# Kernel tuning notes

Hardware: AMD Instinct MI355X
Metric: run time of the kernel (lower is better)

The kernel has to match this reference:

```python
import jax, jax.numpy as jnp
import numpy as np

B, T, F = 256, 128, 256          # batch, input_len, feature_num (= input_size)
HID = [1024, 256]                # hidden_size per layer; HID[-1] must equal F
OUT_LEN = 12
NUM_LAYERS = 2


def setup_inputs() -> dict:
    key = jax.random.key(0)
    ks = jax.random.split(key, 16)
    ins = [F] + HID
    d = {"x": jax.random.normal(ks[0], (B, T, F), dtype=jnp.float32)}
    # Gate order along leading axis 0: [i, f, o, c]
    for j in range(NUM_LAYERS):
        si = 1.0 / np.sqrt(ins[j])
        sh = 1.0 / np.sqrt(HID[j])
        d[f"Wx{j}"] = jax.random.uniform(ks[1 + 4 * j], (4, ins[j], HID[j]), jnp.float32, -si, si)
        d[f"bx{j}"] = jax.random.uniform(ks[2 + 4 * j], (4, HID[j]), jnp.float32, -si, si)
        d[f"Wh{j}"] = jax.random.uniform(ks[3 + 4 * j], (4, HID[j], HID[j]), jnp.float32, -sh, sh)
        d[f"bh{j}"] = jax.random.uniform(ks[4 + 4 * j], (4, HID[j]), jnp.float32, -sh, sh)
    st = 1.0 / np.sqrt(T)
    d["Wout"] = jax.random.uniform(ks[10], (T, OUT_LEN), jnp.float32, -st, st)
    d["bout"] = jax.random.uniform(ks[11], (OUT_LEN,), jnp.float32, -st, st)
    return d


def _lstm_forward(x, Wx, bx, Wh, bh):
    """Stacked LSTM over time. x: (B,T,F). Returns (out_seq (B,T,HID[-1]), h_n list, c_n list)."""
    b = x.shape[0]
    h0 = tuple(jnp.zeros((b, h), x.dtype) for h in HID)
    c0 = tuple(jnp.zeros((b, h), x.dtype) for h in HID)

    def step(carry, x_t):
        hs, cs = carry
        inp = x_t
        new_hs, new_cs = [], []
        for j in range(NUM_LAYERS):
            # fused 4-gate matmuls: (B,in) x (4,in,H) -> (4,B,H)
            g = (jnp.einsum('bi,gih->gbh', inp, Wx[j]) + bx[j][:, None, :]
                 + jnp.einsum('bh,gho->gbo', hs[j], Wh[j]) + bh[j][:, None, :])
            it = jax.nn.sigmoid(g[0])
            ft = jax.nn.sigmoid(g[1])
            ot = jax.nn.sigmoid(g[2])
            c = ft * cs[j] + it * jnp.tanh(g[3])
            h = ot * jnp.tanh(c)
            new_hs.append(h)
            new_cs.append(c)
            inp = h
        return (tuple(new_hs), tuple(new_cs)), inp

    (h_n, c_n), out_seq = jax.lax.scan(step, (h0, c0), jnp.swapaxes(x, 0, 1))
    return jnp.swapaxes(out_seq, 0, 1), h_n, c_n  # (B,T,HID[-1])


def reference(x, Wx0, bx0, Wh0, bh0, Wx1, bx1, Wh1, bh1, Wout, bout):
    Wx = [Wx0, Wx1]; bx = [bx0, bx1]; Wh = [Wh0, Wh1]; bh = [bh0, bh1]
    out_seq, h_n, c_n = _lstm_forward(x, Wx, bx, Wh, bh)
    b = x.shape[0]
    # Faithful to torch: flat row-major view (B,T,F) -> (B,F,T), NOT a transpose
    out = out_seq.reshape(b, -1, T)                 # (B, F, T)
    out = out @ Wout + bout                          # (B, F, OUT_LEN)
    out = out.reshape(b, OUT_LEN, -1)                # (B, OUT_LEN, F)
    return (out, h_n[0], h_n[1], c_n[0], c_n[1])
```

## Files before the change

kernel.cpp:

```cpp
#include <hip/hip_runtime.h>
#include <hip/hip_bf16.h>

typedef unsigned short u16;
typedef unsigned int u32;
typedef unsigned long long u64;
typedef __attribute__((ext_vector_type(8))) short short8;
typedef __attribute__((ext_vector_type(4))) float f32x4;

#define NB 256
#define NT 512
#define TS 128

#define OFF_H0  786432
#define OFF_H1  1048576
#define OFF_C0  1114112
#define OFF_C1  1376256

#define WSO_W0F  0
#define WSO_W1F  (WSO_W0F + 10485760)
#define WSO_B0   (WSO_W1F + 2621440)
#define WSO_B1   (WSO_B0  + 16384)
#define WSO_BAR  (WSO_B1  + 4096)
#define BAR_DW   (4096 + 64)
#define WSO_H0   (WSO_BAR + BAR_DW*4)
#define H0SEQ_BYTES (129*524288)
#define WSO_H1   (WSO_H0 + H0SEQ_BYTES)
#define H1SEQ_BYTES (129*131072)
#define WS_NEED  (WSO_H1 + H1SEQ_BYTES)

#define LDS_XB   65536
#define LDS_B1   98304
#define LDS_SZ   139264

struct MP {
  const float* x;
  const u16*  W0F;
  const u16*  W1F;
  const float* b0;
  const float* b1;
  u16*  H0;
  u16*  H1;
  float* out;
  unsigned* bar;
};

__device__ __forceinline__ float sigm(float x){ return 1.f/(1.f+__expf(-x)); }
__device__ __forceinline__ float tanh_(float x){
  float t = __expf(-2.f*fabsf(x));
  float r = (1.f - t)/(1.f + t);
  return x < 0.f ? -r : r;
}
__device__ __forceinline__ u16 f2b(float v){
  __hip_bfloat16 h = __float2bfloat16(v);
  return *reinterpret_cast<u16*>(&h);
}
__device__ __forceinline__ float b2f(u16 u){
  u32 w = ((u32)u) << 16;
  return *reinterpret_cast<float*>(&w);
}
__device__ __forceinline__ void ast32(u16* p, u32 v){
  __hip_atomic_store((u32*)p, v, __ATOMIC_RELAXED, __HIP_MEMORY_SCOPE_AGENT);
}
__device__ __forceinline__ f32x4 MF(short8 a, short8 b, f32x4 c){
  return __builtin_amdgcn_mfma_f32_16x16x32_bf16(a, b, c, 0, 0, 0);
}
__device__ __forceinline__ void gll16(const void* g, void* l){
  __builtin_amdgcn_global_load_lds(
      (const __attribute__((address_space(1))) void*)g,
      (__attribute__((address_space(3))) void*)l, 16, 0, 0);
}

#define STRX(x) #x
#define PLOADO(dst, ptr, off) asm volatile("global_load_dwordx4 %0, %1, off offset:" STRX(off) : "=v"(dst) : "v"(ptr))
#define VMW(N)  do{ asm volatile("s_waitcnt vmcnt(" STRX(N) ")" ::: "memory"); __builtin_amdgcn_sched_barrier(0); }while(0)
#define BAR     do{ __builtin_amdgcn_s_barrier(); __builtin_amdgcn_sched_barrier(0); }while(0)


__global__ void k_packF0(const float* __restrict__ Wx, const float* __restrict__ Wh,
                         u16* __restrict__ W0F){
  int gid = blockIdx.x*256 + threadIdx.x;
  int F = gid >> 6, lane = gid & 63;
  int kk = F & 3, wn = (F >> 2) & 3;
  int r = F >> 4, kt = r % 10, nt = r / 10;
  int n = nt*64 + wn*16 + (lane & 15);
  int h = n >> 2, g = n & 3;
  int kb = kt*128 + kk*32 + (lane >> 4)*8;
  union { u16 u[8]; short8 v; } pk;
#pragma unroll
  for (int j = 0; j < 8; ++j) {
    int k = kb + j;
    float v = (k < 256) ? Wx[((size_t)g*256 + k)*1024 + h]
                        : Wh[((size_t)g*1024 + (k-256))*1024 + h];
    pk.u[j] = f2b(v);
  }
  *(short8*)&W0F[(size_t)F*512 + lane*8] = pk.v;
}

__global__ void k_packF1(const float* __restrict__ Wx, const float* __restrict__ Wh,
                         u16* __restrict__ W1F){
  int gid = blockIdx.x*256 + threadIdx.x;
  int F = gid >> 6, lane = gid & 63;
  int kk = F & 3, kt = (F >> 2) % 10, ntp = F / 40;
  int n = ntp*16 + (lane & 15);
  int h = n >> 2, g = n & 3;
  int kb = kt*128 + kk*32 + (lane >> 4)*8;
  union { u16 u[8]; short8 v; } pk;
#pragma unroll
  for (int j = 0; j < 8; ++j) {
    int k = kb + j;
    float v = (k < 1024) ? Wx[((size_t)g*1024 + k)*256 + h]
                         : Wh[((size_t)g*256 + (k-1024))*256 + h];
    pk.u[j] = f2b(v);
  }
  *(short8*)&W1F[(size_t)F*512 + lane*8] = pk.v;
}

__global__ void k_bias(const float* __restrict__ bx0, const float* __restrict__ bh0,
                       const float* __restrict__ bx1, const float* __restrict__ bh1,
                       float* __restrict__ b0, float* __restrict__ b1){
  int n = blockIdx.x*256 + threadIdx.x;
  if (n < 4096) { int h = n >> 2, g = n & 3; b0[n] = bx0[g*1024 + h] + bh0[g*1024 + h]; }
  if (n < 1024) { int h = n >> 2, g = n & 3; b1[n] = bx1[g*256 + h] + bh1[g*256 + h]; }
}

__global__ void k_init(u16* __restrict__ H0, u16* __restrict__ H1,
                       unsigned* __restrict__ bar){
  int i = blockIdx.x*256 + threadIdx.x;
  if (i < 262144) H0[i] = 0;
  if (i < 65536)  H1[i] = 0;
  if (i < BAR_DW) bar[i] = 0u;
}


__device__ __forceinline__ void xcvt(const MP& p, int g, char* smem){
  const int tid = threadIdx.x;
  const int row = tid >> 3, f0 = (tid & 7) << 5;
  const int m0 = (blockIdx.x >> 6) << 6;
  const float* xs = p.x + (size_t)(m0 + row)*32768 + (size_t)g*256 + f0;
  f32x4 v0,v1,v2,v3,v4,v5,v6,v7;
  PLOADO(v0, xs, 0);  PLOADO(v1, xs, 16); PLOADO(v2, xs, 32); PLOADO(v3, xs, 48);
  PLOADO(v4, xs, 64); PLOADO(v5, xs, 80); PLOADO(v6, xs, 96); PLOADO(v7, xs, 112);
  VMW(0);
  char* xb = smem + LDS_XB + ((f0 >> 7) << 14);
  const int cb = (f0 & 127) >> 3, sw = row & 7;
  union { u16 u[8]; short8 s; } pk;
#define XPK(VA, VB, CC) \
  pk.u[0]=f2b(VA[0]); pk.u[1]=f2b(VA[1]); pk.u[2]=f2b(VA[2]); pk.u[3]=f2b(VA[3]); \
  pk.u[4]=f2b(VB[0]); pk.u[5]=f2b(VB[1]); pk.u[6]=f2b(VB[2]); pk.u[7]=f2b(VB[3]); \
  *(short8*)(xb + row*256 + ((((cb+(CC)) ^ sw))<<4)) = pk.s;
  XPK(v0,v1,0) XPK(v2,v3,1) XPK(v4,v5,2) XPK(v6,v7,3)
#undef XPK
}

__device__ __forceinline__ void fused(const MP& p, int g, char* smem,
                                      float* c0, float* c1, short8* wp,
                                      bool doP0, bool doP1){
  const int bid = blockIdx.x, tid = threadIdx.x;
  const int grp = bid >> 6, nt = bid & 63;
  const int m0 = grp*64, n0 = nt*64, n1 = nt*16;
  const int lane = tid & 63, wid = tid >> 6;
  const int wm = wid >> 2, wn = wid & 3;
  const int lrow = lane & 15, kgrp = lane >> 4;
  const int sw = lrow & 7;
  const int r8 = lane >> 4, c16 = lane & 15;
  const int row0 = wid*8 + r8, row1 = wid*8 + 4 + r8;
  const char* Hp = (const char*)(p.H0 + (size_t)g*262144);
  const char* h0 = Hp + (size_t)(m0+row0)*2048 + ((c16 ^ (row0 & 7))<<4);
  const char* h1 = Hp + (size_t)(m0+row1)*2048 + ((c16 ^ (row1 & 7))<<4);
  const int gB = (g > 0) ? (g-1) : 0;
  const char* HB = (const char*)(p.H1 + (size_t)gB*65536);
  const char* hB0 = HB + (size_t)(m0+row0)*512 + ((c16 ^ (row0 & 7))<<4);
  const char* hB1 = HB + (size_t)(m0+row1)*512 + ((c16 ^ (row1 & 7))<<4);
  char* d0 = smem + wid*2048;
  char* d1 = smem + wid*2048 + 1024;
  const u16* bb = p.W0F + (size_t)nt*81920 + wn*2048 + lane*8;
  const char* b1p = smem + LDS_B1;

  short8 bx0,bx1,bx2,bx3, by0,by1,by2,by3;
  f32x4 acc0 = {0,0,0,0}, acc1 = {0,0,0,0};
  f32x4 accp = {0,0,0,0};

#define FS0(T) do{ const int _o = ((T)-2)*256, _bi = (((T)-2)&3)*16384; \
    gll16(h0 + _o, d0 + _bi); gll16(h1 + _o, d1 + _bi); }while(0)
#define FS1(T) do{ const int _o = ((T)-10)*256, _bi = (((T)-2)&3)*16384; \
    gll16(hB0 + _o, d0 + _bi); gll16(hB1 + _o, d1 + _bi); }while(0)
#define F_MFB(BP, B0_,B1_,B2_,B3_) do{ const char* _bp = (BP); short8 _a0,_a1; \
    const int _r0 = (wm*32 + lrow)*256, _r1 = _r0 + 16*256; \
    _a0 = *(const short8*)(_bp + _r0 + (((0+kgrp) ^ sw)<<4)); \
    _a1 = *(const short8*)(_bp + _r1 + (((0+kgrp) ^ sw)<<4)); \
    acc0 = MF(_a0,B0_,acc0); acc1 = MF(_a1,B0_,acc1); \
    _a0 = *(const short8*)(_bp + _r0 + (((4+kgrp) ^ sw)<<4)); \
    _a1 = *(const short8*)(_bp + _r1 + (((4+kgrp) ^ sw)<<4)); \
    acc0 = MF(_a0,B1_,acc0); acc1 = MF(_a1,B1_,acc1); \
    _a0 = *(const short8*)(_bp + _r0 + (((8+kgrp) ^ sw)<<4)); \
    _a1 = *(const short8*)(_bp + _r1 + (((8+kgrp) ^ sw)<<4)); \
    acc0 = MF(_a0,B2_,acc0); acc1 = MF(_a1,B2_,acc1); \
    _a0 = *(const short8*)(_bp + _r0 + (((12+kgrp) ^ sw)<<4)); \
    _a1 = *(const short8*)(_bp + _r1 + (((12+kgrp) ^ sw)<<4)); \
    acc0 = MF(_a0,B3_,acc0); acc1 = MF(_a1,B3_,acc1); }while(0)
#define F_MF1(BUFI, KT1) do{ const char* _bp = smem + (BUFI)*16384; \
    const int _ro = (wid*16 + lrow)*256; short8 _a, _b; \
    _a = *(const short8*)(_bp + _ro + (((0+kgrp) ^ sw)<<4)); \
    _b = *(const short8*)(b1p + (((KT1)*4+0)<<10) + lane*16); accp = MF(_a,_b,accp); \
    _a = *(const short8*)(_bp + _ro + (((4+kgrp) ^ sw)<<4)); \
    _b = *(const short8*)(b1p + (((KT1)*4+1)<<10) + lane*16); accp = MF(_a,_b,accp); \
    _a = *(const short8*)(_bp + _ro + (((8+kgrp) ^ sw)<<4)); \
    _b = *(const short8*)(b1p + (((KT1)*4+2)<<10) + lane*16); accp = MF(_a,_b,accp); \
    _a = *(const short8*)(_bp + _ro + (((12+kgrp) ^ sw)<<4)); \
    _b = *(const short8*)(b1p + (((KT1)*4+3)<<10) + lane*16); accp = MF(_a,_b,accp); }while(0)

  { const u16* _s = bb;
    PLOADO(bx0,_s,0); PLOADO(bx1,_s,1024); PLOADO(bx2,_s,2048); PLOADO(bx3,_s,3072); }
  { const u16* _s = bb + 8192;
    PLOADO(by0,_s,0); PLOADO(by1,_s,1024); PLOADO(by2,_s,2048); PLOADO(by3,_s,3072); }
  FS0(2); FS0(3); FS0(4); FS0(5);

  VMW(12); BAR; if (doP0) F_MFB(smem + LDS_XB,         bx0,bx1,bx2,bx3);
  VMW(8);  BAR; if (doP0) F_MFB(smem + LDS_XB + 16384, by0,by1,by2,by3);
  VMW(6); BAR; if (doP0) F_MFB(smem,         wp[0], wp[1], wp[2], wp[3]);
               if (doP1 && wid < 4) F_MF1(0, 0);  FS0(6);
  VMW(6); BAR; if (doP0) F_MFB(smem + 16384, wp[4], wp[5], wp[6], wp[7]);
               if (doP1 && wid < 4) F_MF1(1, 1);  FS0(7);
  VMW(6); BAR; if (doP0) F_MFB(smem + 32768, wp[8], wp[9], wp[10], wp[11]);
               if (doP1 && wid < 4) F_MF1(2, 2);  FS0(8);
  VMW(6); BAR; if (doP0) F_MFB(smem + 49152, wp[12], wp[13], wp[14], wp[15]);
               if (doP1 && wid < 4) F_MF1(3, 3);  FS0(9);
  VMW(6); BAR; if (doP0) F_MFB(smem,         wp[16], wp[17], wp[18], wp[19]);
               if (doP1 && wid < 4) F_MF1(0, 4);  FS1(10);
  VMW(6); BAR; if (doP0) F_MFB(smem + 16384, wp[20], wp[21], wp[22], wp[23]);
               if (doP1 && wid < 4) F_MF1(1, 5);  FS1(11);
  VMW(6); BAR; if (doP0) F_MFB(smem + 32768, wp[24], wp[25], wp[26], wp[27]);
               if (doP1 && wid < 4) F_MF1(2, 6);
  VMW(4); BAR; if (doP0) F_MFB(smem + 49152, wp[28], wp[29], wp[30], wp[31]);
               if (doP1 && wid < 4) F_MF1(3, 7);
  VMW(2); BAR; if (doP1 && wid < 4) F_MF1(0, 8);
  VMW(0); BAR; if (doP1 && wid < 4) F_MF1(1, 9);

  __syncthreads();
  float* gl0 = (float*)smem;
  float* gl1 = (float*)(smem + 20480);
  if (doP0) {
#pragma unroll
    for (int r = 0; r < 4; ++r) {
      gl0[(wm*32      + kgrp*4 + r)*68 + wn*16 + lrow] = acc0[r];
      gl0[(wm*32 + 16 + kgrp*4 + r)*68 + wn*16 + lrow] = acc1[r];
    }
  }
  if (doP1 && wid < 4) {
#pragma unroll
    for (int r = 0; r < 4; ++r)
      gl1[(wid*16 + kgrp*4 + r)*20 + lrow] = accp[r];
  }
  __syncthreads();
  if (doP0) {
    u16* H0w = p.H0 + (size_t)(g+1)*262144;
    int bl = tid >> 3, hp = tid & 7;
    int b = m0 + bl, h = nt*16 + hp*2;
    float hn[2];
#pragma unroll
    for (int q = 0; q < 2; ++q) {
      int col = (hp*2 + q)*4;
      float gi = gl0[bl*68 + col+0] + p.b0[n0 + col+0];
      float gf = gl0[bl*68 + col+1] + p.b0[n0 + col+1];
      float go = gl0[bl*68 + col+2] + p.b0[n0 + col+2];
      float gc = gl0[bl*68 + col+3] + p.b0[n0 + col+3];
      float cn = sigm(gf)*c0[q] + sigm(gi)*tanh_(gc);
      hn[q] = sigm(go)*tanh_(cn);
      c0[q] = cn;
      if (g == TS-1) {
        p.out[OFF_H0 + (size_t)b*1024 + h + q] = hn[q];
        p.out[OFF_C0 + (size_t)b*1024 + h + q] = cn;
      }
    }
    ast32(H0w + (size_t)b*1024 + h, (u32)f2b(hn[0]) | ((u32)f2b(hn[1]) << 16));
  }
  if (doP1 && tid < 128) {
    u16* H1w = p.H1 + (size_t)g*65536;
    int bl = tid >> 1, hp = tid & 1;
    int b = m0 + bl, h = nt*4 + hp*2;
    float hn[2];
#pragma unroll
    for (int q = 0; q < 2; ++q) {
      int col = (hp*2 + q)*4;
      float gi = gl1[bl*20 + col+0] + p.b1[n1 + col+0];
      float gf = gl1[bl*20 + col+1] + p.b1[n1 + col+1];
      float go = gl1[bl*20 + col+2] + p.b1[n1 + col+2];
      float gc = gl1[bl*20 + col+3] + p.b1[n1 + col+3];
      float cn = sigm(gf)*c1[q] + sigm(gi)*tanh_(gc);
      hn[q] = sigm(go)*tanh_(cn);
      c1[q] = cn;
      if (g == TS) {
        p.out[OFF_H1 + (size_t)b*256 + h + q] = hn[q];
        p.out[OFF_C1 + (size_t)b*256 + h + q] = cn;
      }
    }
    ast32(H1w + (size_t)b*256 + h, (u32)f2b(hn[0]) | ((u32)f2b(hn[1]) << 16));
  }
}

__global__ __launch_bounds__(NT, 1) void k_main(MP p){
  __shared__ __attribute__((aligned(16))) char smem[LDS_SZ];
  float c0[2] = {0.f, 0.f};
  float c1[2] = {0.f, 0.f};
  short8 wp[32];
  const int bid = blockIdx.x, tid = threadIdx.x;
  const int grp = bid >> 6, j = bid & 63;
  const int lane = tid & 63, wid = tid >> 6;
  unsigned* flags = p.bar;
  unsigned* rel   = p.bar + 4096 + grp*16;

  {
    const char* wsrc = (const char*)p.W1F + (size_t)j*40960 + lane*16;
#pragma unroll
    for (int q = 0; q < 5; ++q) {
      int f = wid*5 + q;
      gll16(wsrc + f*1024, smem + LDS_B1 + f*1024);
    }
    VMW(0);
  }
  {
    const u16* bb = p.W0F + (size_t)j*81920 + (wid & 3)*2048 + lane*8;
#define LDW(T) do{ const u16* _s = bb + (size_t)(T)*8192; \
    PLOADO(wp[((T)-2)*4+0],_s,0); PLOADO(wp[((T)-2)*4+1],_s,1024); \
    PLOADO(wp[((T)-2)*4+2],_s,2048); PLOADO(wp[((T)-2)*4+3],_s,3072); }while(0)
    LDW(2); LDW(3); LDW(4); LDW(5); LDW(6); LDW(7); LDW(8); LDW(9);
#undef LDW
    VMW(0);
  }

  xcvt(p, 0, smem);
  __syncthreads();
  fused(p, 0, smem, c0, c1, wp, true, false);

  for (int g = 1; g <= TS; ++g) {
    __syncthreads();
    if (j == 0) {
      if (tid >= 1 && tid < 64) {
        while (__hip_atomic_load(&flags[(grp*64 + tid)*16], __ATOMIC_RELAXED,
                                 __HIP_MEMORY_SCOPE_AGENT) < (unsigned)g)
          __builtin_amdgcn_s_sleep(1);
      }
      __syncthreads();
      if (tid == 0)
        __hip_atomic_store(rel, (unsigned)g, __ATOMIC_RELAXED, __HIP_MEMORY_SCOPE_AGENT);
    } else {
      if (tid == 0)
        __hip_atomic_store(&flags[bid*16], (unsigned)g, __ATOMIC_RELAXED,
                           __HIP_MEMORY_SCOPE_AGENT);
    }
    if (g < TS) xcvt(p, g, smem);
    if (j != 0 && tid == 0) {
      while (__hip_atomic_load(rel, __ATOMIC_RELAXED, __HIP_MEMORY_SCOPE_AGENT) < (unsigned)g)
        __builtin_amdgcn_s_sleep(1);
    }
    __syncthreads();
    fused(p, g, smem, c0, c1, wp, g < TS, true);
  }
}

__global__ void k_final_seq(const u16* __restrict__ H1seq, const float* __restrict__ Wout,
                            const float* __restrict__ bout, float* __restrict__ out){
  __shared__ float Ws[1536];
  __shared__ float bs[12];
  for (int i = threadIdx.x; i < 1536; i += 256) Ws[i] = Wout[i];
  if (threadIdx.x < 12) bs[threadIdx.x] = bout[threadIdx.x];
  __syncthreads();
  int gid = blockIdx.x*256 + threadIdx.x;
  int b = gid >> 8, ii = gid & 255;
  const u16* src = H1seq + (size_t)((ii >> 1) + 1)*65536 + b*256 + (ii & 1)*128;
  float acc[12];
#pragma unroll
  for (int k = 0; k < 12; ++k) acc[k] = bs[k];
  for (int jj = 0; jj < 128; jj += 8) {
    union { u16 u[8]; short8 v; } pk;
    pk.v = *(const short8*)&src[jj];
#pragma unroll
    for (int e = 0; e < 8; ++e) {
      float f = b2f(pk.u[e]);
#pragma unroll
      for (int k = 0; k < 12; ++k) acc[k] += f*Ws[(jj+e)*12+k];
    }
  }
  float* dst = out + (size_t)b*3072 + ii*12;
#pragma unroll
  for (int k = 0; k < 12; ++k) dst[k] = acc[k];
}

extern "C" void kernel_launch(void* const* d_in, const int* in_sizes, int n_in,
                              void* d_out, int out_size, void* d_ws, size_t ws_size,
                              hipStream_t stream) {
  if (ws_size < (size_t)WS_NEED) return;
  const float* x    = (const float*)d_in[0];
  const float* Wx0  = (const float*)d_in[1];
  const float* bx0  = (const float*)d_in[2];
  const float* Wh0  = (const float*)d_in[3];
  const float* bh0  = (const float*)d_in[4];
  const float* Wx1  = (const float*)d_in[5];
  const float* bx1  = (const float*)d_in[6];
  const float* Wh1  = (const float*)d_in[7];
  const float* bh1  = (const float*)d_in[8];
  const float* Wout = (const float*)d_in[9];
  const float* bout = (const float*)d_in[10];

  char* ws = (char*)d_ws;
  u16*   W0F  = (u16*)  (ws + WSO_W0F);
  u16*   W1F  = (u16*)  (ws + WSO_W1F);
  float* b0   = (float*)(ws + WSO_B0);
  float* b1   = (float*)(ws + WSO_B1);
  unsigned* bar = (unsigned*)(ws + WSO_BAR);
  u16*   H0   = (u16*)  (ws + WSO_H0);
  u16*   H1   = (u16*)  (ws + WSO_H1);
  float* out = (float*)d_out;

  k_packF0<<<2560, 256, 0, stream>>>(Wx0, Wh0, W0F);
  k_packF1<<<640, 256, 0, stream>>>(Wx1, Wh1, W1F);
  k_bias<<<16, 256, 0, stream>>>(bx0, bh0, bx1, bh1, b0, b1);
  k_init<<<1024, 256, 0, stream>>>(H0, H1, bar);

  MP p;
  p.x = x; p.W0F = W0F; p.W1F = W1F; p.b0 = b0; p.b1 = b1;
  p.H0 = H0; p.H1 = H1; p.out = out; p.bar = bar;
  void* kargs[] = { (void*)&p };
  hipLaunchCooperativeKernel((const void*)k_main, dim3(NB), dim3(NT), kargs, 0, stream);

  k_final_seq<<<256, 256, 0, stream>>>(H1, Wout, bout, out);
}
```

Measured before the change: 1.205 ms.

## Keep x-projection weights in registers and pipeline H loads with six LDS buffers

The layer-0 input-projection weight fragments (first two k-tiles) now stay in registers for the whole run instead of being reloaded from global memory every timestep. The x tile is written to the start of LDS, and the recurrent H loads now rotate through six 16KB buffers, two k-tiles per barrier stage. This halves the number of barriers and vmcnt waits per step. In exchange it costs more VGPRs (eight extra short8 per thread) and uses more LDS buffer space.

```diff
diff --git a/kernel.cpp b/kernel.cpp
--- a/kernel.cpp
+++ b/kernel.cpp
@@ -28,7 +28,6 @@
 #define H1SEQ_BYTES (129*131072)
 #define WS_NEED  (WSO_H1 + H1SEQ_BYTES)
 
-#define LDS_XB   65536
 #define LDS_B1   98304
 #define LDS_SZ   139264
 
@@ -141,7 +140,7 @@
   PLOADO(v0, xs, 0);  PLOADO(v1, xs, 16); PLOADO(v2, xs, 32); PLOADO(v3, xs, 48);
   PLOADO(v4, xs, 64); PLOADO(v5, xs, 80); PLOADO(v6, xs, 96); PLOADO(v7, xs, 112);
   VMW(0);
-  char* xb = smem + LDS_XB + ((f0 >> 7) << 14);
+  char* xb = smem + ((f0 >> 7) << 14);
   const int cb = (f0 & 127) >> 3, sw = row & 7;
   union { u16 u[8]; short8 s; } pk;
 #define XPK(VA, VB, CC) \
@@ -153,7 +152,8 @@
 }
 
 __device__ __forceinline__ void fused(const MP& p, int g, char* smem,
-                                      float* c0, float* c1, short8* wp,
+                                      float* c0, float* c1,
+                                      short8* wp, short8* wpx,
                                       bool doP0, bool doP1){
   const int bid = blockIdx.x, tid = threadIdx.x;
   const int grp = bid >> 6, nt = bid & 63;
@@ -173,16 +173,14 @@
   const char* hB1 = HB + (size_t)(m0+row1)*512 + ((c16 ^ (row1 & 7))<<4);
   char* d0 = smem + wid*2048;
   char* d1 = smem + wid*2048 + 1024;
-  const u16* bb = p.W0F + (size_t)nt*81920 + wn*2048 + lane*8;
   const char* b1p = smem + LDS_B1;
 
-  short8 bx0,bx1,bx2,bx3, by0,by1,by2,by3;
   f32x4 acc0 = {0,0,0,0}, acc1 = {0,0,0,0};
   f32x4 accp = {0,0,0,0};
 
-#define FS0(T) do{ const int _o = ((T)-2)*256, _bi = (((T)-2)&3)*16384; \
+#define FS0(T) do{ const int _o = ((T)-2)*256, _bi = ((T)%6)*16384; \
     gll16(h0 + _o, d0 + _bi); gll16(h1 + _o, d1 + _bi); }while(0)
-#define FS1(T) do{ const int _o = ((T)-10)*256, _bi = (((T)-2)&3)*16384; \
+#define FS1(T) do{ const int _o = ((T)-10)*256, _bi = ((T)%6)*16384; \
     gll16(hB0 + _o, d0 + _bi); gll16(hB1 + _o, d1 + _bi); }while(0)
 #define F_MFB(BP, B0_,B1_,B2_,B3_) do{ const char* _bp = (BP); short8 _a0,_a1; \
     const int _r0 = (wm*32 + lrow)*256, _r1 = _r0 + 16*256; \
@@ -198,7 +196,7 @@
     _a0 = *(const short8*)(_bp + _r0 + (((12+kgrp) ^ sw)<<4)); \
     _a1 = *(const short8*)(_bp + _r1 + (((12+kgrp) ^ sw)<<4)); \
     acc0 = MF(_a0,B3_,acc0); acc1 = MF(_a1,B3_,acc1); }while(0)
-#define F_MF1(BUFI, KT1) do{ const char* _bp = smem + (BUFI)*16384; \
+#define F_MF1(BP, KT1) do{ const char* _bp = (BP); \
     const int _ro = (wid*16 + lrow)*256; short8 _a, _b; \
     _a = *(const short8*)(_bp + _ro + (((0+kgrp) ^ sw)<<4)); \
     _b = *(const short8*)(b1p + (((KT1)*4+0)<<10) + lane*16); accp = MF(_a,_b,accp); \
@@ -209,32 +207,33 @@
     _a = *(const short8*)(_bp + _ro + (((12+kgrp) ^ sw)<<4)); \
     _b = *(const short8*)(b1p + (((KT1)*4+3)<<10) + lane*16); accp = MF(_a,_b,accp); }while(0)
 
-  { const u16* _s = bb;
-    PLOADO(bx0,_s,0); PLOADO(bx1,_s,1024); PLOADO(bx2,_s,2048); PLOADO(bx3,_s,3072); }
-  { const u16* _s = bb + 8192;
-    PLOADO(by0,_s,0); PLOADO(by1,_s,1024); PLOADO(by2,_s,2048); PLOADO(by3,_s,3072); }
   FS0(2); FS0(3); FS0(4); FS0(5);
 
-  VMW(12); BAR; if (doP0) F_MFB(smem + LDS_XB,         bx0,bx1,bx2,bx3);
-  VMW(8);  BAR; if (doP0) F_MFB(smem + LDS_XB + 16384, by0,by1,by2,by3);
-  VMW(6); BAR; if (doP0) F_MFB(smem,         wp[0], wp[1], wp[2], wp[3]);
-               if (doP1 && wid < 4) F_MF1(0, 0);  FS0(6);
-  VMW(6); BAR; if (doP0) F_MFB(smem + 16384, wp[4], wp[5], wp[6], wp[7]);
-               if (doP1 && wid < 4) F_MF1(1, 1);  FS0(7);
-  VMW(6); BAR; if (doP0) F_MFB(smem + 32768, wp[8], wp[9], wp[10], wp[11]);
-               if (doP1 && wid < 4) F_MF1(2, 2);  FS0(8);
-  VMW(6); BAR; if (doP0) F_MFB(smem + 49152, wp[12], wp[13], wp[14], wp[15]);
-               if (doP1 && wid < 4) F_MF1(3, 3);  FS0(9);
-  VMW(6); BAR; if (doP0) F_MFB(smem,         wp[16], wp[17], wp[18], wp[19]);
-               if (doP1 && wid < 4) F_MF1(0, 4);  FS1(10);
-  VMW(6); BAR; if (doP0) F_MFB(smem + 16384, wp[20], wp[21], wp[22], wp[23]);
-               if (doP1 && wid < 4) F_MF1(1, 5);  FS1(11);
-  VMW(6); BAR; if (doP0) F_MFB(smem + 32768, wp[24], wp[25], wp[26], wp[27]);
-               if (doP1 && wid < 4) F_MF1(2, 6);
-  VMW(4); BAR; if (doP0) F_MFB(smem + 49152, wp[28], wp[29], wp[30], wp[31]);
-               if (doP1 && wid < 4) F_MF1(3, 7);
-  VMW(2); BAR; if (doP1 && wid < 4) F_MF1(0, 8);
-  VMW(0); BAR; if (doP1 && wid < 4) F_MF1(1, 9);
+  if (doP0) {
+    F_MFB(smem,         wpx[0], wpx[1], wpx[2], wpx[3]);
+    F_MFB(smem + 16384, wpx[4], wpx[5], wpx[6], wpx[7]);
+  }
+  VMW(4); BAR;
+  FS0(6); FS0(7);
+  if (doP0) { F_MFB(smem + 32768, wp[0], wp[1], wp[2], wp[3]);
+              F_MFB(smem + 49152, wp[4], wp[5], wp[6], wp[7]); }
+  if (doP1 && wid < 4) { F_MF1(smem + 32768, 0); F_MF1(smem + 49152, 1); }
+  VMW(4); BAR;
+  FS0(8); FS0(9);
+  if (doP0) { F_MFB(smem + 65536, wp[8], wp[9], wp[10], wp[11]);
+              F_MFB(smem + 81920, wp[12], wp[13], wp[14], wp[15]); }
+  if (doP1 && wid < 4) { F_MF1(smem + 65536, 2); F_MF1(smem + 81920, 3); }
+  VMW(4); BAR;
+  FS1(10); FS1(11);
+  if (doP0) { F_MFB(smem,         wp[16], wp[17], wp[18], wp[19]);
+              F_MFB(smem + 16384, wp[20], wp[21], wp[22], wp[23]); }
+  if (doP1 && wid < 4) { F_MF1(smem, 4); F_MF1(smem + 16384, 5); }
+  VMW(4); BAR;
+  if (doP0) { F_MFB(smem + 32768, wp[24], wp[25], wp[26], wp[27]);
+              F_MFB(smem + 49152, wp[28], wp[29], wp[30], wp[31]); }
+  if (doP1 && wid < 4) { F_MF1(smem + 32768, 6); F_MF1(smem + 49152, 7); }
+  VMW(0); BAR;
+  if (doP1 && wid < 4) { F_MF1(smem + 65536, 8); F_MF1(smem + 81920, 9); }
 
   __syncthreads();
   float* gl0 = (float*)smem;
@@ -303,6 +302,7 @@
   float c0[2] = {0.f, 0.f};
   float c1[2] = {0.f, 0.f};
   short8 wp[32];
+  short8 wpx[8];
   const int bid = blockIdx.x, tid = threadIdx.x;
   const int grp = bid >> 6, j = bid & 63;
   const int lane = tid & 63, wid = tid >> 6;
@@ -320,6 +320,11 @@
   }
   {
     const u16* bb = p.W0F + (size_t)j*81920 + (wid & 3)*2048 + lane*8;
+#define LDWX(T) do{ const u16* _s = bb + (size_t)(T)*8192; \
+    PLOADO(wpx[(T)*4+0],_s,0); PLOADO(wpx[(T)*4+1],_s,1024); \
+    PLOADO(wpx[(T)*4+2],_s,2048); PLOADO(wpx[(T)*4+3],_s,3072); }while(0)
+    LDWX(0); LDWX(1);
+#undef LDWX
 #define LDW(T) do{ const u16* _s = bb + (size_t)(T)*8192; \
     PLOADO(wp[((T)-2)*4+0],_s,0); PLOADO(wp[((T)-2)*4+1],_s,1024); \
     PLOADO(wp[((T)-2)*4+2],_s,2048); PLOADO(wp[((T)-2)*4+3],_s,3072); }while(0)
@@ -330,7 +335,7 @@
 
   xcvt(p, 0, smem);
   __syncthreads();
-  fused(p, 0, smem, c0, c1, wp, true, false);
+  fused(p, 0, smem, c0, c1, wp, wpx, true, false);
 
   for (int g = 1; g <= TS; ++g) {
     __syncthreads();
@@ -354,7 +359,7 @@
         __builtin_amdgcn_s_sleep(1);
     }
     __syncthreads();
-    fused(p, g, smem, c0, c1, wp, g < TS, true);
+    fused(p, g, smem, c0, c1, wp, wpx, g < TS, true);
   }
 }
 
```

After: 1.295 ms. +7.5%, slower.
